# Optimization experiments

Hardware: AMD Instinct MI355X
Metric: run time of the kernel (lower is better)

The kernel has to match this reference:

```python
import jax, jax.numpy as jnp
import numpy as np

IN_DIMS = (8, 16, 8)
EMBED = 1024
HEADS = 16
HEAD_DIM = EMBED // HEADS
RANK = 16
CORE_SHAPES = [(1, 8, 8, RANK), (RANK, 16, 16, RANK), (RANK, 8, 8, 1)]


def tt_linear(x, cores, bias):
    """Apply a TT-matrix to x: [N, prod(IN_DIMS)] -> [N, prod(out_dims)].

    Cores G_k: [r_{k-1}, i_k, o_k, r_k], r_0 = r_d = 1. Sequential chain of
    small rank-bounded contractions, faithful to TTLinear.forward.
    """
    N = x.shape[0]
    t = x.reshape(N, 1, 1, -1)  # (N, O_done, r, I_rest)
    for G, i in zip(cores, IN_DIMS):
        rest = t.shape[-1] // i
        t = t.reshape(N, t.shape[1], t.shape[2], i, rest)
        # contract input mode i and left rank r -> output mode q and right rank s
        t = jnp.einsum('norik,riqs->noqsk', t, G)
        t = t.reshape(N, t.shape[1] * t.shape[2], t.shape[3], -1)
    return t.reshape(N, -1) + bias


def setup_inputs() -> dict:
    key = jax.random.key(0)
    ks = iter(jax.random.split(key, 32))
    inp = {"query": jax.random.normal(next(ks), (2, 2048, EMBED), dtype=jnp.float32)}
    for name in ("wq", "wk", "wv", "wo"):
        for ci, shp in enumerate(CORE_SHAPES):
            inp[f"{name}_c{ci}"] = jax.random.normal(next(ks), shp, dtype=jnp.float32) * 0.3
        inp[f"{name}_b"] = jax.random.normal(next(ks), (EMBED,), dtype=jnp.float32) * 0.02
    return inp


def reference(query, wq_c0, wq_c1, wq_c2, wq_b, wk_c0, wk_c1, wk_c2, wk_b,
              wv_c0, wv_c1, wv_c2, wv_b, wo_c0, wo_c1, wo_c2, wo_b):
    B, Lq, _ = query.shape
    flat = query.reshape(-1, EMBED)
    # self-attention: key = value = query
    Q = tt_linear(flat, (wq_c0, wq_c1, wq_c2), wq_b).reshape(B, Lq, HEADS, HEAD_DIM)
    K = tt_linear(flat, (wk_c0, wk_c1, wk_c2), wk_b).reshape(B, Lq, HEADS, HEAD_DIM)
    V = tt_linear(flat, (wv_c0, wv_c1, wv_c2), wv_b).reshape(B, Lq, HEADS, HEAD_DIM)
    Q = Q.transpose(0, 2, 1, 3)  # bhqd
    K = K.transpose(0, 2, 1, 3)
    V = V.transpose(0, 2, 1, 3)
    scale = HEAD_DIM ** -0.5
    scores = jnp.einsum('bhqd,bhkd->bhqk', Q, K) * scale
    attn = jax.nn.softmax(scores, axis=-1)
    ctx = jnp.einsum('bhqk,bhkd->bhqd', attn, V)
    ctx = ctx.transpose(0, 2, 1, 3).reshape(B * Lq, EMBED)
    out = tt_linear(ctx, (wo_c0, wo_c1, wo_c2), wo_b)
    return out.reshape(B, Lq, EMBED)
```

## Files before the change

### kernel.cpp

```cpp
#include <hip/hip_runtime.h>
#include <hip/hip_bf16.h>
#include <stdint.h>

#define LQ 2048
#define NTOK 4096

typedef __attribute__((ext_vector_type(8))) short short8;
typedef __attribute__((ext_vector_type(4))) float f32x4;
typedef __attribute__((ext_vector_type(16))) float f32x16;
typedef __attribute__((ext_vector_type(4))) unsigned short u16x4;

#define MFMA16(a, b, c) __builtin_amdgcn_mfma_f32_16x16x32_bf16((a), (b), (c), 0, 0, 0)
#define MFMA32(a, b, c) __builtin_amdgcn_mfma_f32_32x32x16_bf16((a), (b), (c), 0, 0, 0)

__device__ __forceinline__ unsigned short f2bf(float x) {
    union { __hip_bfloat16 b; unsigned short u; } v;
    v.b = __float2bfloat16(x);
    return v.u;
}
__device__ __forceinline__ float bf2f(unsigned short h) {
    union { uint32_t u; float f; } v; v.u = ((uint32_t)h) << 16; return v.f;
}
__device__ __forceinline__ unsigned int cvtpk_bf16(float lo, float hi_) {
    unsigned int r;
    asm("v_cvt_pk_bf16_f32 %0, %1, %2" : "=v"(r) : "v"(lo), "v"(hi_));
    return r;
}
__device__ __forceinline__ void permswap(unsigned int &a, unsigned int &b) {
    asm("v_permlane32_swap_b32 %0, %1" : "+v"(a), "+v"(b));
}
__device__ __forceinline__ float fast_exp2(float x) {
    float r;
    asm("v_exp_f32 %0, %1" : "=v"(r) : "v"(x));
    return r;
}

struct CorePtrs {
    const float* c0[4];
    const float* c1[4];
    const float* c2[4];
};

struct QkvOut {
    unsigned short* hi[3];
    unsigned short* lo[2];
    const float* bias[3];
    float osc[3];
};

__global__ __launch_bounds__(256) void build_w_kernel(
    CorePtrs cp, unsigned short* __restrict__ Whi, unsigned short* __restrict__ Wlo)
{
    __shared__ float B1[16 * 16 * 16];
    const int p  = blockIdx.y;
    const int i0 = blockIdx.x >> 3;
    const int q0 = blockIdx.x & 7;
    const int t  = threadIdx.x;
    const float* __restrict__ c0 = cp.c0[p];
    const float* __restrict__ c1 = cp.c1[p];
    const float* __restrict__ c2 = cp.c2[p];

    float g0[16];
#pragma unroll
    for (int s = 0; s < 16; ++s) g0[s] = c0[(i0 * 8 + q0) * 16 + s];

    for (int idx = t; idx < 4096; idx += 256) {
        const int s2 = idx & 15;
        const int q1 = (idx >> 4) & 15;
        const int i1 = idx >> 8;
        float acc = 0.f;
#pragma unroll
        for (int s = 0; s < 16; ++s)
            acc += g0[s] * c1[((s * 16 + i1) * 16 + q1) * 16 + s2];
        B1[idx] = acc;
    }
    __syncthreads();

    const size_t base = (size_t)p * 1024 * 1024;
    for (int idx = t; idx < 16384; idx += 256) {
        const int q2 = idx & 7;
        const int i2 = (idx >> 3) & 7;
        const int q1 = (idx >> 6) & 15;
        const int i1 = idx >> 10;
        float acc = 0.f;
#pragma unroll
        for (int s2 = 0; s2 < 16; ++s2)
            acc += B1[(i1 * 16 + q1) * 16 + s2] * c2[(s2 * 8 + i2) * 8 + q2];
        const int o = q0 * 128 + q1 * 8 + q2;
        const int e = i0 * 128 + i1 * 8 + i2;
        const unsigned short hi = f2bf(acc);
        Whi[base + o * 1024 + e] = hi;
        Wlo[base + o * 1024 + e] = f2bf(acc - bf2f(hi));
    }
}

__global__ __launch_bounds__(256) void convert_x_kernel(
    const float* __restrict__ X, unsigned short* __restrict__ Xhi,
    unsigned short* __restrict__ Xlo, int n4)
{
    const int i = blockIdx.x * 256 + threadIdx.x;
    if (i >= n4) return;
    const float4 v = ((const float4*)X)[i];
    u16x4 hi, lo;
    float vv[4] = {v.x, v.y, v.z, v.w};
#pragma unroll
    for (int j = 0; j < 4; ++j) {
        unsigned short h = f2bf(vv[j]);
        hi[j] = h;
        lo[j] = f2bf(vv[j] - bf2f(h));
    }
    ((u16x4*)Xhi)[i] = hi;
    ((u16x4*)Xlo)[i] = lo;
}

__global__ __launch_bounds__(256) void gemm_qkv_kernel(
    const unsigned short* __restrict__ Xh, const unsigned short* __restrict__ Xl,
    const unsigned short* __restrict__ Wh, const unsigned short* __restrict__ Wl,
    QkvOut op)
{
    __shared__ unsigned short Ah[128 * 32];
    __shared__ unsigned short Bh[128 * 32];
    __shared__ unsigned short Al[128 * 32];
    __shared__ unsigned short Bl[128 * 32];

    const int t = threadIdx.x;
    const int l = t & 63;
    const int w = t >> 6;
    const int wr = (w >> 1) * 64, wc = (w & 1) * 64;
    const int bm = blockIdx.y * 128, bn = blockIdx.x * 128;
    const bool is_v = (bn >> 10) == 2;

    f32x4 acc[4][4];
#pragma unroll
    for (int i = 0; i < 4; ++i)
#pragma unroll
        for (int j = 0; j < 4; ++j) acc[i][j] = (f32x4){0.f, 0.f, 0.f, 0.f};

    const int srow = t >> 1;
    const int sch  = (t & 1) * 2;
    const int ssel = (srow >> 1) & 3;
    const int sd0  = srow * 32 + (((sch)     ^ ssel) << 3);
    const int sd1  = srow * 32 + (((sch + 1) ^ ssel) << 3);
    const size_t xoff = (size_t)(bm + srow) * 1024 + sch * 8;
    const size_t woff = (size_t)(bn + srow) * 1024 + sch * 8;

    const int fsel = ((l & 15) >> 1) & 3;
    const int fpos = ((l >> 4) ^ fsel) << 3;
    const int fra  = (wr + (l & 15)) * 32 + fpos;
    const int frb  = (wc + (l & 15)) * 32 + fpos;

    short8 pXh0, pXh1, pWh0, pWh1, pXl0, pXl1, pWl0, pWl1;
    pXh0 = *(const short8*)&Xh[xoff];     pXh1 = *(const short8*)&Xh[xoff + 8];
    pWh0 = *(const short8*)&Wh[woff];     pWh1 = *(const short8*)&Wh[woff + 8];
    if (!is_v) {
        pXl0 = *(const short8*)&Xl[xoff]; pXl1 = *(const short8*)&Xl[xoff + 8];
        pWl0 = *(const short8*)&Wl[woff]; pWl1 = *(const short8*)&Wl[woff + 8];
    }

    for (int e0 = 0; e0 < 1024; e0 += 32) {
        __syncthreads();
        *(short8*)&Ah[sd0] = pXh0; *(short8*)&Ah[sd1] = pXh1;
        *(short8*)&Bh[sd0] = pWh0; *(short8*)&Bh[sd1] = pWh1;
        if (!is_v) {
            *(short8*)&Al[sd0] = pXl0; *(short8*)&Al[sd1] = pXl1;
            *(short8*)&Bl[sd0] = pWl0; *(short8*)&Bl[sd1] = pWl1;
        }
        __syncthreads();

        if (e0 + 32 < 1024) {
            const size_t xo = xoff + e0 + 32, wo = woff + e0 + 32;
            pXh0 = *(const short8*)&Xh[xo];     pXh1 = *(const short8*)&Xh[xo + 8];
            pWh0 = *(const short8*)&Wh[wo];     pWh1 = *(const short8*)&Wh[wo + 8];
            if (!is_v) {
                pXl0 = *(const short8*)&Xl[xo]; pXl1 = *(const short8*)&Xl[xo + 8];
                pWl0 = *(const short8*)&Wl[wo]; pWl1 = *(const short8*)&Wl[wo + 8];
            }
        }

        short8 af[4], bfv[4], afl[4], bfl[4];
#pragma unroll
        for (int rb = 0; rb < 4; ++rb) {
            af[rb]  = *(const short8*)&Ah[fra + rb * 512];
            bfv[rb] = *(const short8*)&Bh[frb + rb * 512];
        }
#pragma unroll
        for (int rb = 0; rb < 4; ++rb)
#pragma unroll
            for (int cb = 0; cb < 4; ++cb)
                acc[rb][cb] = MFMA16(af[rb], bfv[cb], acc[rb][cb]);
        if (!is_v) {
#pragma unroll
            for (int rb = 0; rb < 4; ++rb) afl[rb] = *(const short8*)&Al[fra + rb * 512];
#pragma unroll
            for (int rb = 0; rb < 4; ++rb)
#pragma unroll
                for (int cb = 0; cb < 4; ++cb)
                    acc[rb][cb] = MFMA16(afl[rb], bfv[cb], acc[rb][cb]);
#pragma unroll
            for (int rb = 0; rb < 4; ++rb) bfl[rb] = *(const short8*)&Bl[frb + rb * 512];
#pragma unroll
            for (int rb = 0; rb < 4; ++rb)
#pragma unroll
                for (int cb = 0; cb < 4; ++cb)
                    acc[rb][cb] = MFMA16(af[rb], bfl[cb], acc[rb][cb]);
        }
    }

    const int p = bn >> 10;
    unsigned short* __restrict__ yh = op.hi[p];
    unsigned short* __restrict__ yl = (p < 2) ? op.lo[p] : nullptr;
    const float* __restrict__ bp = op.bias[p];
    const float osc = op.osc[p];
    const int bnl = bn & 1023;

    const int r0 = (l >> 4) * 4;
    const int cc = l & 15;
#pragma unroll
    for (int rb = 0; rb < 4; ++rb)
#pragma unroll
        for (int cb = 0; cb < 4; ++cb) {
            const int col = bnl + wc + cb * 16 + cc;
            const float bv = bp[col];
#pragma unroll
            for (int r = 0; r < 4; ++r) {
                const int row = bm + wr + rb * 16 + r0 + r;
                const float v = (acc[rb][cb][r] + bv) * osc;
                const unsigned short hi = f2bf(v);
                yh[(size_t)row * 1024 + col] = hi;
                if (p < 2)
                    yl[(size_t)row * 1024 + col] = f2bf(v - bf2f(hi));
            }
        }
}

__global__ __launch_bounds__(256) void gemm_out_kernel(
    const unsigned short* __restrict__ Xh,
    const unsigned short* __restrict__ Wh,
    const float* __restrict__ bias,
    float* __restrict__ Yf)
{
    __shared__ unsigned short Ah[64 * 32];
    __shared__ unsigned short Bh[128 * 32];

    const int t = threadIdx.x;
    const int l = t & 63;
    const int w = t >> 6;
    const int wr = (w >> 1) * 32, wc = (w & 1) * 64;
    const int bm = blockIdx.y * 64, bn = blockIdx.x * 128;

    f32x4 acc[2][4];
#pragma unroll
    for (int i = 0; i < 2; ++i)
#pragma unroll
        for (int j = 0; j < 4; ++j) acc[i][j] = (f32x4){0.f, 0.f, 0.f, 0.f};

    const int arow = t >> 2, ach = t & 3;
    const int asd  = arow * 32 + ((ach ^ ((arow >> 1) & 3)) << 3);
    const size_t xoff = (size_t)(bm + arow) * 1024 + ach * 8;
    const int brow = t >> 1, bch = (t & 1) * 2;
    const int bsel = (brow >> 1) & 3;
    const int bsd0 = brow * 32 + (((bch)     ^ bsel) << 3);
    const int bsd1 = brow * 32 + (((bch + 1) ^ bsel) << 3);
    const size_t woff = (size_t)(bn + brow) * 1024 + bch * 8;

    const int fsel = ((l & 15) >> 1) & 3;
    const int fpos = ((l >> 4) ^ fsel) << 3;
    const int fra  = (wr + (l & 15)) * 32 + fpos;
    const int frb  = (wc + (l & 15)) * 32 + fpos;

    short8 pA0, pB0, pB1;
    pA0 = *(const short8*)&Xh[xoff];
    pB0 = *(const short8*)&Wh[woff]; pB1 = *(const short8*)&Wh[woff + 8];

    for (int e0 = 0; e0 < 1024; e0 += 32) {
        __syncthreads();
        *(short8*)&Ah[asd]  = pA0;
        *(short8*)&Bh[bsd0] = pB0; *(short8*)&Bh[bsd1] = pB1;
        __syncthreads();

        if (e0 + 32 < 1024) {
            pA0 = *(const short8*)&Xh[xoff + e0 + 32];
            pB0 = *(const short8*)&Wh[woff + e0 + 32];
            pB1 = *(const short8*)&Wh[woff + e0 + 40];
        }

        short8 af[2], bfv[4];
#pragma unroll
        for (int rb = 0; rb < 2; ++rb) af[rb] = *(const short8*)&Ah[fra + rb * 512];
#pragma unroll
        for (int cb = 0; cb < 4; ++cb) bfv[cb] = *(const short8*)&Bh[frb + cb * 512];
#pragma unroll
        for (int rb = 0; rb < 2; ++rb)
#pragma unroll
            for (int cb = 0; cb < 4; ++cb)
                acc[rb][cb] = MFMA16(af[rb], bfv[cb], acc[rb][cb]);
    }

    const int r0 = (l >> 4) * 4;
    const int cc = l & 15;
#pragma unroll
    for (int rb = 0; rb < 2; ++rb)
#pragma unroll
        for (int cb = 0; cb < 4; ++cb) {
            const int col = bn + wc + cb * 16 + cc;
            const float bv = bias[col];
#pragma unroll
            for (int r = 0; r < 4; ++r) {
                const int row = bm + wr + rb * 16 + r0 + r;
                Yf[(size_t)row * 1024 + col] = acc[rb][cb][r] + bv;
            }
        }
}

__global__ __launch_bounds__(256) void transpose_kernel(
    const unsigned short* __restrict__ V, unsigned short* __restrict__ VT)
{
    __shared__ unsigned short tile[64][65];
    const int t = threadIdx.x;
    const int c0 = blockIdx.x * 64;
    const int r0 = blockIdx.y * 64;
    {
        const int r = t >> 2;
        const int q = (t & 3) * 16;
        short8 v0 = *(const short8*)&V[(size_t)(r0 + r) * 1024 + c0 + q];
        short8 v1 = *(const short8*)&V[(size_t)(r0 + r) * 1024 + c0 + q + 8];
#pragma unroll
        for (int i = 0; i < 8; ++i) {
            tile[r][q + i]     = (unsigned short)v0[i];
            tile[r][q + 8 + i] = (unsigned short)v1[i];
        }
    }
    __syncthreads();
    {
        const int c = t >> 2;
        const int g = (t & 3) * 16;
        short8 out0, out1;
#pragma unroll
        for (int i = 0; i < 8; ++i) {
            out0[i] = (short)tile[g + i][c];
            out1[i] = (short)tile[g + 8 + i][c];
        }
        *(short8*)&VT[(size_t)(c0 + c) * 4096 + r0 + g]     = out0;
        *(short8*)&VT[(size_t)(c0 + c) * 4096 + r0 + g + 8] = out1;
    }
}

__global__ __launch_bounds__(256) void attn_kernel(
    const unsigned short* __restrict__ Qh, const unsigned short* __restrict__ Ql,
    const unsigned short* __restrict__ Kh_g, const unsigned short* __restrict__ Kl_g,
    const unsigned short* __restrict__ VT, unsigned short* __restrict__ CTX)
{
    __shared__ unsigned short Khs[2][64 * 64];
    __shared__ unsigned short Kls[2][64 * 64];
    __shared__ unsigned short Vts[2][64 * 64];

    const int t = threadIdx.x;
    const int l = t & 63;
    const int w = t >> 6;
    const int qt = blockIdx.x, h = blockIdx.y, b = blockIdx.z;
    const int lq = l & 31;
    const int hi = l >> 5;
    const int tokq = b * LQ + qt * 128 + w * 32;

    short8 qhf[4], qlf[4];
    {
        const size_t qr = (size_t)(tokq + lq) * 1024 + h * 64 + hi * 8;
#pragma unroll
        for (int ds = 0; ds < 4; ++ds) {
            qhf[ds] = *(const short8*)&Qh[qr + ds * 16];
            qlf[ds] = *(const short8*)&Ql[qr + ds * 16];
        }
    }

    f32x16 o0, o1;
#pragma unroll
    for (int i = 0; i < 16; ++i) { o0[i] = 0.f; o1[i] = 0.f; }
    float m = -1e30f, lsum = 0.f;

    const int srow = t >> 2;
    const int sch  = (t & 3) * 2;
    int sdst[2];
#pragma unroll
    for (int it = 0; it < 2; ++it)
        sdst[it] = srow * 64 + (((sch + it) ^ (srow & 7)) << 3);

    const unsigned short* pkh = Kh_g + (size_t)(b * LQ + srow) * 1024 + h * 64 + sch * 8;
    const unsigned short* pkl = Kl_g + (size_t)(b * LQ + srow) * 1024 + h * 64 + sch * 8;
    const unsigned short* pvt = VT + (size_t)(h * 64 + srow) * 4096 + b * LQ + sch * 8;

    short8 pf_kh[2], pf_kl[2], pf_vt[2];
    pf_kh[0] = *(const short8*)pkh;       pf_kh[1] = *(const short8*)(pkh + 8);
    pf_kl[0] = *(const short8*)pkl;       pf_kl[1] = *(const short8*)(pkl + 8);
    pf_vt[0] = *(const short8*)pvt;       pf_vt[1] = *(const short8*)(pvt + 8);

    const int lq7 = lq & 7;
    int qkoff[4], pvslot[4];
#pragma unroll
    for (int i = 0; i < 4; ++i) {
        qkoff[i]  = lq * 64 + (((2 * i + hi) ^ lq7) << 3);
        pvslot[i] = (((2 * i + hi) ^ lq7) << 3);
    }

    int cur = 0;
    for (int kt = 0; kt < 32; ++kt) {
#pragma unroll
        for (int it = 0; it < 2; ++it) {
            *(short8*)&Khs[cur][sdst[it]] = pf_kh[it];
            *(short8*)&Kls[cur][sdst[it]] = pf_kl[it];
            *(short8*)&Vts[cur][sdst[it]] = pf_vt[it];
        }
        if (kt < 31) {
            pkh += 64 * 1024; pkl += 64 * 1024; pvt += 64;
            pf_kh[0] = *(const short8*)pkh;  pf_kh[1] = *(const short8*)(pkh + 8);
            pf_kl[0] = *(const short8*)pkl;  pf_kl[1] = *(const short8*)(pkl + 8);
            pf_vt[0] = *(const short8*)pvt;  pf_vt[1] = *(const short8*)(pvt + 8);
        }
        __syncthreads();

        f32x16 s0, s1;
#pragma unroll
        for (int i = 0; i < 16; ++i) { s0[i] = 0.f; s1[i] = 0.f; }
        __builtin_amdgcn_s_setprio(1);
#pragma unroll
        for (int ds = 0; ds < 4; ++ds) {
            const int off = qkoff[ds];
            short8 kh0 = *(const short8*)&Khs[cur][off];
            short8 kh1 = *(const short8*)&Khs[cur][off + 2048];
            short8 kl0 = *(const short8*)&Kls[cur][off];
            short8 kl1 = *(const short8*)&Kls[cur][off + 2048];
            s0 = MFMA32(kh0, qhf[ds], s0);
            s1 = MFMA32(kh1, qhf[ds], s1);
            s0 = MFMA32(kl0, qhf[ds], s0);
            s1 = MFMA32(kl1, qhf[ds], s1);
            s0 = MFMA32(kh0, qlf[ds], s0);
            s1 = MFMA32(kh1, qlf[ds], s1);
        }
        __builtin_amdgcn_s_setprio(0);

        float vm = fmaxf(fmaxf(s0[0], s0[1]), s0[2]);
#pragma unroll
        for (int i = 3; i < 15; i += 2) vm = fmaxf(fmaxf(s0[i], s0[i + 1]), vm);
        vm = fmaxf(fmaxf(s0[15], s1[0]), vm);
#pragma unroll
        for (int i = 1; i < 15; i += 2) vm = fmaxf(fmaxf(s1[i], s1[i + 1]), vm);
        vm = fmaxf(s1[15], vm);
        vm = fmaxf(vm, __shfl_xor(vm, 32));
        const float mg = fmaxf(m, vm);
        if (__any(mg > m + 8.f)) {
            const float mu = (mg > m + 8.f) ? mg : m;
            const float alpha = fast_exp2(m - mu);
            lsum *= alpha;
            o0 *= alpha;
            o1 *= alpha;
            m = mu;
        }
        float ps = 0.f;
#pragma unroll
        for (int i = 0; i < 16; ++i) { s0[i] = fast_exp2(s0[i] - m); ps += s0[i]; }
#pragma unroll
        for (int i = 0; i < 16; ++i) { s1[i] = fast_exp2(s1[i] - m); ps += s1[i]; }
        lsum += ps;

        unsigned int pw[4][4];
        {
            unsigned int a, bb;
            a = cvtpk_bf16(s0[0], s0[1]); bb = cvtpk_bf16(s0[4], s0[5]);
            permswap(a, bb); pw[0][0] = a; pw[0][2] = bb;
            a = cvtpk_bf16(s0[2], s0[3]); bb = cvtpk_bf16(s0[6], s0[7]);
            permswap(a, bb); pw[0][1] = a; pw[0][3] = bb;
            a = cvtpk_bf16(s0[8], s0[9]); bb = cvtpk_bf16(s0[12], s0[13]);
            permswap(a, bb); pw[1][0] = a; pw[1][2] = bb;
            a = cvtpk_bf16(s0[10], s0[11]); bb = cvtpk_bf16(s0[14], s0[15]);
            permswap(a, bb); pw[1][1] = a; pw[1][3] = bb;
            a = cvtpk_bf16(s1[0], s1[1]); bb = cvtpk_bf16(s1[4], s1[5]);
            permswap(a, bb); pw[2][0] = a; pw[2][2] = bb;
            a = cvtpk_bf16(s1[2], s1[3]); bb = cvtpk_bf16(s1[6], s1[7]);
            permswap(a, bb); pw[2][1] = a; pw[2][3] = bb;
            a = cvtpk_bf16(s1[8], s1[9]); bb = cvtpk_bf16(s1[12], s1[13]);
            permswap(a, bb); pw[3][0] = a; pw[3][2] = bb;
            a = cvtpk_bf16(s1[10], s1[11]); bb = cvtpk_bf16(s1[14], s1[15]);
            permswap(a, bb); pw[3][1] = a; pw[3][3] = bb;
        }

        __builtin_amdgcn_s_setprio(1);
#pragma unroll
        for (int ks = 0; ks < 4; ++ks) {
            union { unsigned int u[4]; short8 v; } pa;
            pa.u[0] = pw[ks][0]; pa.u[1] = pw[ks][1];
            pa.u[2] = pw[ks][2]; pa.u[3] = pw[ks][3];
            const int slot = pvslot[ks];
            short8 v0 = *(const short8*)&Vts[cur][lq * 64 + slot];
            short8 v1 = *(const short8*)&Vts[cur][(32 + lq) * 64 + slot];
            o0 = MFMA32(v0, pa.v, o0);
            o1 = MFMA32(v1, pa.v, o1);
        }
        __builtin_amdgcn_s_setprio(0);
        cur ^= 1;
    }

    lsum += __shfl_xor(lsum, 32);
    const float inv = 1.f / lsum;
    const size_t orow = (size_t)(tokq + lq) * 1024 + h * 64 + hi * 4;
#pragma unroll
    for (int g = 0; g < 4; ++g) {
        u16x4 pack0, pack1;
#pragma unroll
        for (int j = 0; j < 4; ++j) {
            pack0[j] = f2bf(o0[4 * g + j] * inv);
            pack1[j] = f2bf(o1[4 * g + j] * inv);
        }
        *(u16x4*)&CTX[orow + 8 * g]      = pack0;
        *(u16x4*)&CTX[orow + 32 + 8 * g] = pack1;
    }
}

extern "C" void kernel_launch(void* const* d_in, const int* in_sizes, int n_in,
                              void* d_out, int out_size, void* d_ws, size_t ws_size,
                              hipStream_t stream)
{
    (void)in_sizes; (void)n_in; (void)out_size; (void)ws_size;
    const float* query = (const float*)d_in[0];
    char* base = (char*)d_ws;
    const size_t MB = 1 << 20;
    unsigned short* Whi = (unsigned short*)(base + 0 * MB);
    unsigned short* Wlo = (unsigned short*)(base + 8 * MB);
    unsigned short* Xhi = (unsigned short*)(base + 16 * MB);
    unsigned short* Xlo = (unsigned short*)(base + 24 * MB);
    unsigned short* Qhi = (unsigned short*)(base + 32 * MB);
    unsigned short* Qlo = (unsigned short*)(base + 40 * MB);
    unsigned short* Khi = (unsigned short*)(base + 48 * MB);
    unsigned short* Klo = (unsigned short*)(base + 56 * MB);
    unsigned short* Vh  = (unsigned short*)(base + 64 * MB);
    unsigned short* VTp = (unsigned short*)(base + 72 * MB);
    unsigned short* CTX = (unsigned short*)(base + 16 * MB);

    CorePtrs cp;
    for (int p = 0; p < 4; ++p) {
        cp.c0[p] = (const float*)d_in[1 + 4 * p];
        cp.c1[p] = (const float*)d_in[2 + 4 * p];
        cp.c2[p] = (const float*)d_in[3 + 4 * p];
    }
    const size_t WSZ = (size_t)1024 * 1024;
    const float QSCALE = 0.125f * 1.44269504088896340736f;

    build_w_kernel<<<dim3(64, 4), 256, 0, stream>>>(cp, Whi, Wlo);
    convert_x_kernel<<<4096, 256, 0, stream>>>(query, Xhi, Xlo, 1048576);

    QkvOut op;
    op.hi[0] = Qhi; op.hi[1] = Khi; op.hi[2] = Vh;
    op.lo[0] = Qlo; op.lo[1] = Klo;
    op.bias[0] = (const float*)d_in[4];
    op.bias[1] = (const float*)d_in[8];
    op.bias[2] = (const float*)d_in[12];
    op.osc[0] = QSCALE; op.osc[1] = 1.0f; op.osc[2] = 1.0f;

    gemm_qkv_kernel<<<dim3(24, 32), 256, 0, stream>>>(Xhi, Xlo, Whi, Wlo, op);

    transpose_kernel<<<dim3(16, 64), 256, 0, stream>>>(Vh, VTp);

    attn_kernel<<<dim3(16, 16, 2), 256, 0, stream>>>(Qhi, Qlo, Khi, Klo, VTp, CTX);

    gemm_out_kernel<<<dim3(8, 64), 256, 0, stream>>>(
        CTX, Whi + 3 * WSZ, (const float*)d_in[16], (float*)d_out);
}
```

Baseline: 285.3 us.

## Fuse weight build with input conversion, write V transposed from QKV GEMM epilogue

The separate weight-build and input-conversion kernels are merged into one prep kernel launch. The QKV GEMM epilogue now writes V directly in transposed layout, which removes the standalone transpose kernel and its round trip through memory. In the attention kernel, the max and exp-sum reductions are split across several independent accumulators to shorten dependency chains. The transposed V stores are 8-byte writes at a stride of 4096 elements per column, so they may coalesce poorly.

```diff
diff --git a/kernel.cpp b/kernel.cpp
--- a/kernel.cpp
+++ b/kernel.cpp
@@ -42,20 +42,41 @@
 };
 
 struct QkvOut {
-    unsigned short* hi[3];
-    unsigned short* lo[2];
+    unsigned short* qhi;
+    unsigned short* qlo;
+    unsigned short* khi;
+    unsigned short* klo;
+    unsigned short* vt;
     const float* bias[3];
-    float osc[3];
+    float qscale;
 };
 
-__global__ __launch_bounds__(256) void build_w_kernel(
-    CorePtrs cp, unsigned short* __restrict__ Whi, unsigned short* __restrict__ Wlo)
+__global__ __launch_bounds__(256) void prep_kernel(
+    CorePtrs cp, unsigned short* __restrict__ Whi, unsigned short* __restrict__ Wlo,
+    const float* __restrict__ X, unsigned short* __restrict__ Xhi,
+    unsigned short* __restrict__ Xlo)
 {
+    const int blk = blockIdx.x;
+    const int t = threadIdx.x;
+    if (blk >= 256) {
+        const int i = (blk - 256) * 256 + t;
+        const float4 v = ((const float4*)X)[i];
+        u16x4 hi, lo;
+        float vv[4] = {v.x, v.y, v.z, v.w};
+#pragma unroll
+        for (int j = 0; j < 4; ++j) {
+            unsigned short h = f2bf(vv[j]);
+            hi[j] = h;
+            lo[j] = f2bf(vv[j] - bf2f(h));
+        }
+        ((u16x4*)Xhi)[i] = hi;
+        ((u16x4*)Xlo)[i] = lo;
+        return;
+    }
     __shared__ float B1[16 * 16 * 16];
-    const int p  = blockIdx.y;
-    const int i0 = blockIdx.x >> 3;
-    const int q0 = blockIdx.x & 7;
-    const int t  = threadIdx.x;
+    const int p  = blk >> 6;
+    const int i0 = (blk & 63) >> 3;
+    const int q0 = blk & 7;
     const float* __restrict__ c0 = cp.c0[p];
     const float* __restrict__ c1 = cp.c1[p];
     const float* __restrict__ c2 = cp.c2[p];
@@ -92,25 +113,6 @@
         Whi[base + o * 1024 + e] = hi;
         Wlo[base + o * 1024 + e] = f2bf(acc - bf2f(hi));
     }
-}
-
-__global__ __launch_bounds__(256) void convert_x_kernel(
-    const float* __restrict__ X, unsigned short* __restrict__ Xhi,
-    unsigned short* __restrict__ Xlo, int n4)
-{
-    const int i = blockIdx.x * 256 + threadIdx.x;
-    if (i >= n4) return;
-    const float4 v = ((const float4*)X)[i];
-    u16x4 hi, lo;
-    float vv[4] = {v.x, v.y, v.z, v.w};
-#pragma unroll
-    for (int j = 0; j < 4; ++j) {
-        unsigned short h = f2bf(vv[j]);
-        hi[j] = h;
-        lo[j] = f2bf(vv[j] - bf2f(h));
-    }
-    ((u16x4*)Xhi)[i] = hi;
-    ((u16x4*)Xlo)[i] = lo;
 }
 
 __global__ __launch_bounds__(256) void gemm_qkv_kernel(
@@ -207,30 +209,46 @@
     }
 
     const int p = bn >> 10;
-    unsigned short* __restrict__ yh = op.hi[p];
-    unsigned short* __restrict__ yl = (p < 2) ? op.lo[p] : nullptr;
     const float* __restrict__ bp = op.bias[p];
-    const float osc = op.osc[p];
     const int bnl = bn & 1023;
-
     const int r0 = (l >> 4) * 4;
     const int cc = l & 15;
-#pragma unroll
-    for (int rb = 0; rb < 4; ++rb)
-#pragma unroll
-        for (int cb = 0; cb < 4; ++cb) {
-            const int col = bnl + wc + cb * 16 + cc;
-            const float bv = bp[col];
-#pragma unroll
-            for (int r = 0; r < 4; ++r) {
-                const int row = bm + wr + rb * 16 + r0 + r;
-                const float v = (acc[rb][cb][r] + bv) * osc;
-                const unsigned short hi = f2bf(v);
-                yh[(size_t)row * 1024 + col] = hi;
-                if (p < 2)
+
+    if (p < 2) {
+        unsigned short* __restrict__ yh = (p == 0) ? op.qhi : op.khi;
+        unsigned short* __restrict__ yl = (p == 0) ? op.qlo : op.klo;
+        const float osc = (p == 0) ? op.qscale : 1.0f;
+#pragma unroll
+        for (int rb = 0; rb < 4; ++rb)
+#pragma unroll
+            for (int cb = 0; cb < 4; ++cb) {
+                const int col = bnl + wc + cb * 16 + cc;
+                const float bv = bp[col];
+#pragma unroll
+                for (int r = 0; r < 4; ++r) {
+                    const int row = bm + wr + rb * 16 + r0 + r;
+                    const float v = (acc[rb][cb][r] + bv) * osc;
+                    const unsigned short hi = f2bf(v);
+                    yh[(size_t)row * 1024 + col] = hi;
                     yl[(size_t)row * 1024 + col] = f2bf(v - bf2f(hi));
+                }
             }
-        }
+    } else {
+        unsigned short* __restrict__ vt = op.vt;
+#pragma unroll
+        for (int rb = 0; rb < 4; ++rb)
+#pragma unroll
+            for (int cb = 0; cb < 4; ++cb) {
+                const int col = bnl + wc + cb * 16 + cc;
+                const float bv = bp[col];
+                u16x4 pk;
+#pragma unroll
+                for (int r = 0; r < 4; ++r)
+                    pk[r] = f2bf(acc[rb][cb][r] + bv);
+                const int row0 = bm + wr + rb * 16 + r0;
+                *(u16x4*)&vt[(size_t)col * 4096 + row0] = pk;
+            }
+    }
 }
 
 __global__ __launch_bounds__(256) void gemm_out_kernel(
@@ -310,39 +328,6 @@
                 Yf[(size_t)row * 1024 + col] = acc[rb][cb][r] + bv;
             }
         }
-}
-
-__global__ __launch_bounds__(256) void transpose_kernel(
-    const unsigned short* __restrict__ V, unsigned short* __restrict__ VT)
-{
-    __shared__ unsigned short tile[64][65];
-    const int t = threadIdx.x;
-    const int c0 = blockIdx.x * 64;
-    const int r0 = blockIdx.y * 64;
-    {
-        const int r = t >> 2;
-        const int q = (t & 3) * 16;
-        short8 v0 = *(const short8*)&V[(size_t)(r0 + r) * 1024 + c0 + q];
-        short8 v1 = *(const short8*)&V[(size_t)(r0 + r) * 1024 + c0 + q + 8];
-#pragma unroll
-        for (int i = 0; i < 8; ++i) {
-            tile[r][q + i]     = (unsigned short)v0[i];
-            tile[r][q + 8 + i] = (unsigned short)v1[i];
-        }
-    }
-    __syncthreads();
-    {
-        const int c = t >> 2;
-        const int g = (t & 3) * 16;
-        short8 out0, out1;
-#pragma unroll
-        for (int i = 0; i < 8; ++i) {
-            out0[i] = (short)tile[g + i][c];
-            out1[i] = (short)tile[g + 8 + i][c];
-        }
-        *(short8*)&VT[(size_t)(c0 + c) * 4096 + r0 + g]     = out0;
-        *(short8*)&VT[(size_t)(c0 + c) * 4096 + r0 + g + 8] = out1;
-    }
 }
 
 __global__ __launch_bounds__(256) void attn_kernel(
@@ -437,13 +422,19 @@
         }
         __builtin_amdgcn_s_setprio(0);
 
-        float vm = fmaxf(fmaxf(s0[0], s0[1]), s0[2]);
-#pragma unroll
-        for (int i = 3; i < 15; i += 2) vm = fmaxf(fmaxf(s0[i], s0[i + 1]), vm);
-        vm = fmaxf(fmaxf(s0[15], s1[0]), vm);
-#pragma unroll
-        for (int i = 1; i < 15; i += 2) vm = fmaxf(fmaxf(s1[i], s1[i + 1]), vm);
-        vm = fmaxf(s1[15], vm);
+        float v0 = fmaxf(s0[0], s0[1]), v1 = fmaxf(s0[2], s0[3]);
+        float v2 = fmaxf(s0[4], s0[5]), v3 = fmaxf(s0[6], s0[7]);
+#pragma unroll
+        for (int i = 8; i < 16; i += 4) {
+            v0 = fmaxf(v0, fmaxf(s0[i], s0[i + 1]));
+            v1 = fmaxf(v1, fmaxf(s0[i + 2], s0[i + 3]));
+        }
+#pragma unroll
+        for (int i = 0; i < 16; i += 4) {
+            v2 = fmaxf(v2, fmaxf(s1[i], s1[i + 1]));
+            v3 = fmaxf(v3, fmaxf(s1[i + 2], s1[i + 3]));
+        }
+        float vm = fmaxf(fmaxf(v0, v1), fmaxf(v2, v3));
         vm = fmaxf(vm, __shfl_xor(vm, 32));
         const float mg = fmaxf(m, vm);
         if (__any(mg > m + 8.f)) {
@@ -454,12 +445,22 @@
             o1 *= alpha;
             m = mu;
         }
-        float ps = 0.f;
-#pragma unroll
-        for (int i = 0; i < 16; ++i) { s0[i] = fast_exp2(s0[i] - m); ps += s0[i]; }
-#pragma unroll
-        for (int i = 0; i < 16; ++i) { s1[i] = fast_exp2(s1[i] - m); ps += s1[i]; }
-        lsum += ps;
+        float p0 = 0.f, p1 = 0.f, p2 = 0.f, p3 = 0.f;
+#pragma unroll
+        for (int i = 0; i < 16; i += 4) {
+            s0[i]     = fast_exp2(s0[i] - m);     p0 += s0[i];
+            s0[i + 1] = fast_exp2(s0[i + 1] - m); p1 += s0[i + 1];
+            s0[i + 2] = fast_exp2(s0[i + 2] - m); p2 += s0[i + 2];
+            s0[i + 3] = fast_exp2(s0[i + 3] - m); p3 += s0[i + 3];
+        }
+#pragma unroll
+        for (int i = 0; i < 16; i += 4) {
+            s1[i]     = fast_exp2(s1[i] - m);     p0 += s1[i];
+            s1[i + 1] = fast_exp2(s1[i + 1] - m); p1 += s1[i + 1];
+            s1[i + 2] = fast_exp2(s1[i + 2] - m); p2 += s1[i + 2];
+            s1[i + 3] = fast_exp2(s1[i + 3] - m); p3 += s1[i + 3];
+        }
+        lsum += (p0 + p1) + (p2 + p3);
 
         unsigned int pw[4][4];
         {
@@ -489,10 +490,10 @@
             pa.u[0] = pw[ks][0]; pa.u[1] = pw[ks][1];
             pa.u[2] = pw[ks][2]; pa.u[3] = pw[ks][3];
             const int slot = pvslot[ks];
-            short8 v0 = *(const short8*)&Vts[cur][lq * 64 + slot];
-            short8 v1 = *(const short8*)&Vts[cur][(32 + lq) * 64 + slot];
-            o0 = MFMA32(v0, pa.v, o0);
-            o1 = MFMA32(v1, pa.v, o1);
+            short8 va = *(const short8*)&Vts[cur][lq * 64 + slot];
+            short8 vb = *(const short8*)&Vts[cur][(32 + lq) * 64 + slot];
+            o0 = MFMA32(va, pa.v, o0);
+            o1 = MFMA32(vb, pa.v, o1);
         }
         __builtin_amdgcn_s_setprio(0);
         cur ^= 1;
@@ -530,7 +531,6 @@
     unsigned short* Qlo = (unsigned short*)(base + 40 * MB);
     unsigned short* Khi = (unsigned short*)(base + 48 * MB);
     unsigned short* Klo = (unsigned short*)(base + 56 * MB);
-    unsigned short* Vh  = (unsigned short*)(base + 64 * MB);
     unsigned short* VTp = (unsigned short*)(base + 72 * MB);
     unsigned short* CTX = (unsigned short*)(base + 16 * MB);
 
@@ -543,20 +543,15 @@
     const size_t WSZ = (size_t)1024 * 1024;
     const float QSCALE = 0.125f * 1.44269504088896340736f;
 
-    build_w_kernel<<<dim3(64, 4), 256, 0, stream>>>(cp, Whi, Wlo);
-    convert_x_kernel<<<4096, 256, 0, stream>>>(query, Xhi, Xlo, 1048576);
+    prep_kernel<<<4352, 256, 0, stream>>>(cp, Whi, Wlo, query, Xhi, Xlo);
 
     QkvOut op;
-    op.hi[0] = Qhi; op.hi[1] = Khi; op.hi[2] = Vh;
-    op.lo[0] = Qlo; op.lo[1] = Klo;
+    op.qhi = Qhi; op.qlo = Qlo; op.khi = Khi; op.klo = Klo; op.vt = VTp;
     op.bias[0] = (const float*)d_in[4];
     op.bias[1] = (const float*)d_in[8];
     op.bias[2] = (const float*)d_in[12];
-    op.osc[0] = QSCALE; op.osc[1] = 1.0f; op.osc[2] = 1.0f;
-
+    op.qscale = QSCALE;
     gemm_qkv_kernel<<<dim3(24, 32), 256, 0, stream>>>(Xhi, Xlo, Whi, Wlo, op);
-
-    transpose_kernel<<<dim3(16, 64), 256, 0, stream>>>(Vh, VTp);
 
     attn_kernel<<<dim3(16, 16, 2), 256, 0, stream>>>(Qhi, Qlo, Khi, Klo, VTp, CTX);
 
```

New measurement: 275.1 us. 3.6% less time.
